# Kernel optimization log

Measured on AMD Instinct MI355X. Metric: run time of the kernel, lower is better.

## Reference

```python
import jax, jax.numpy as jnp
import numpy as np

# Model dims
D = 64          # node channels (dim)
M = 16          # msg_channels
DEPTH = 3
VOCAB = 21      # num_atom_tokens
N = 100000      # nodes
E = 1600000     # directed edges
EIN = 2 * D + 1            # edge_mlp input: [x_i, x_j, |rel|^2]
EH = 2 * EIN               # dim_expansion * edge_input_dim
CH = 4 * M                 # 2 * dim_expansion * msg_channels
NH = 2 * D                 # dim_expansion * in_channels
INIT_STD = 1e-3            # init_eps normal init for Linear weights


def setup_inputs() -> dict:
    key = jax.random.key(0)
    ks = jax.random.split(key, 16)
    feats = jax.random.randint(ks[0], (N,), 0, VOCAB, dtype=jnp.int32)
    coors = jax.random.normal(ks[1], (N, 3), dtype=jnp.float32) * 10.0
    edge_index = jax.random.randint(ks[2], (2, E), 0, N, dtype=jnp.int32)
    emb = jax.random.normal(ks[3], (VOCAB, D), dtype=jnp.float32) * 0.1
    f32 = jnp.float32
    return {
        "feats": feats, "coors": coors, "edge_index": edge_index, "emb": emb,
        # edge_mlp: Linear(EIN->EH), SiLU, Linear(EH->M), SiLU
        "We1": jax.random.normal(ks[4], (DEPTH, EIN, EH), f32) * INIT_STD,
        "be1": jnp.zeros((DEPTH, EH), f32),
        "We2": jax.random.normal(ks[5], (DEPTH, EH, M), f32) * INIT_STD,
        "be2": jnp.zeros((DEPTH, M), f32),
        # coord_mlp: Linear(M->CH), SiLU, Linear(CH->1)
        "Wc1": jax.random.normal(ks[6], (DEPTH, M, CH), f32) * INIT_STD,
        "bc1": jnp.zeros((DEPTH, CH), f32),
        "Wc2": jax.random.normal(ks[7], (DEPTH, CH, 1), f32) * INIT_STD,
        "bc2": jnp.zeros((DEPTH, 1), f32),
        # node_mlp: Linear(D+M->NH), SiLU, Linear(NH->D)
        "Wn1": jax.random.normal(ks[8], (DEPTH, D + M, NH), f32) * INIT_STD,
        "bn1": jnp.zeros((DEPTH, NH), f32),
        "Wn2": jax.random.normal(ks[9], (DEPTH, NH, D), f32) * INIT_STD,
        "bn2": jnp.zeros((DEPTH, D), f32),
    }


def reference(feats, coors, edge_index, emb,
              We1, be1, We2, be2, Wc1, bc1, Wc2, bc2, Wn1, bn1, Wn2, bn2):
    # node_encoder: embedding lookup
    x = emb[feats]                       # [N, D]
    pos = coors                          # [N, 3]
    src = edge_index[0]                  # x_j / pos_j (source, flow source->target)
    tgt = edge_index[1]                  # x_i / pos_i (target) = scatter index
    n = x.shape[0]
    for l in range(DEPTH):
        # message: per-edge gather + MLPs
        rel = pos[tgt] - pos[src]                              # [E, 3]
        d2 = jnp.sum(rel * rel, axis=1, keepdims=True)         # [E, 1]
        m_in = jnp.concatenate([x[tgt], x[src], d2], axis=1)   # [E, 2D+1]
        h = jax.nn.silu(m_in @ We1[l] + be1[l])                # [E, EH]
        msg = jax.nn.silu(h @ We2[l] + be2[l])                 # [E, M]
        cw = jax.nn.silu(msg @ Wc1[l] + bc1[l]) @ Wc2[l] + bc2[l]  # [E, 1]
        pos_msg = rel * cw                                     # [E, 3] (coors_norm is Identity)
        # aggregate: scatter-add to target nodes
        agg_msg = jax.ops.segment_sum(msg, tgt, num_segments=n)      # [N, M]
        agg_pos = jax.ops.segment_sum(pos_msg, tgt, num_segments=n)  # [N, 3]
        # node update: node_norm is Identity
        nh = jax.nn.silu(jnp.concatenate([x, agg_msg], axis=1) @ Wn1[l] + bn1[l])
        out_x = nh @ Wn2[l] + bn2[l]                           # [N, D]
        pos = pos + agg_pos                                    # out_pos += pos (no velocity)
        x = x + out_x                                          # residual=True
    return x, pos
```

## Files before the change

### kernel.cpp

```cpp
#include <hip/hip_runtime.h>
#include <hip/hip_bf16.h>
#include <stdint.h>

#define NDIM   64
#define MDIM   16
#define NLAYER 3
#define EIN    129
#define EHD    258
#define CHD    64
#define NHD    128
#define NIN    80
#define AB_STRIDE 512
#define PKT_STRIDE 32
#define FP8_SCALE 1024.0f
#define NVALS  19

#define WE1F_L (34*2*512)
#define WN1F_L (8*3*512)
#define WN2F_L (4*4*512)
#define WE2F_L (9*512)
#define WC1F_L (4*512)

typedef float vf2 __attribute__((ext_vector_type(2)));
typedef __bf16 bf16x8 __attribute__((ext_vector_type(8)));
typedef float  f32x4  __attribute__((ext_vector_type(4)));

#define MFMA16(a, b, c) __builtin_amdgcn_mfma_f32_16x16x32_bf16((a), (b), (c), 0, 0, 0)

__device__ __forceinline__ float rcp_f(float x) { return __builtin_amdgcn_rcpf(x); }
#if __has_builtin(__builtin_amdgcn_exp2f)
__device__ __forceinline__ float exp2_f(float x) { return __builtin_amdgcn_exp2f(x); }
#else
__device__ __forceinline__ float exp2_f(float x) { return __expf(x * 0.6931471805599453f); }
#endif
__device__ __forceinline__ float silu_f(float v) {
    return v * rcp_f(1.0f + __expf(-v));
}
#define CC_EXP (-1.4426950408889634f / 1024.0f)
__device__ __forceinline__ float hprime_f(float u) {
    return u * rcp_f(1.0f + exp2_f(CC_EXP * u));
}
__device__ __forceinline__ float bflo(uint32_t u) {
    union { uint32_t u; float f; } c; c.u = u << 16; return c.f;
}
__device__ __forceinline__ float bfhi(uint32_t u) {
    union { uint32_t u; float f; } c; c.u = u & 0xffff0000u; return c.f;
}
__device__ __forceinline__ uint32_t pk_fp8_4(float f0, float f1, float f2, float f3) {
    uint32_t r = (uint32_t)__builtin_amdgcn_cvt_pk_fp8_f32(f0, f1, 0, false);
    r = (uint32_t)__builtin_amdgcn_cvt_pk_fp8_f32(f2, f3, (int)r, true);
    return r;
}
__device__ __forceinline__ float clamp8(float v) {
    return fminf(448.0f, fmaxf(-448.0f, v * FP8_SCALE));
}

__global__ void prep_kernel(const float* __restrict__ We1, const float* __restrict__ Wn1,
                            const float* __restrict__ Wn2, const float* __restrict__ We2,
                            const float* __restrict__ Wc1,
                            __bf16* __restrict__ WE1F, __bf16* __restrict__ WN1F,
                            __bf16* __restrict__ WN2F, __bf16* __restrict__ WE2F,
                            __bf16* __restrict__ WC1F) {
    int idx = blockIdx.x * 256 + threadIdx.x;
    const int T1 = NLAYER * WE1F_L;
    if (idx < T1) {
        int l  = idx / WE1F_L;
        int r  = idx % WE1F_L;
        int ct = r / 1024;
        int r2 = r % 1024;
        int kh = r2 / 512;
        int r3 = r2 % 512;
        int lane = r3 >> 3, jj = r3 & 7;
        int half = ct / 17, ctl = ct % 17;
        int col = ctl * 16 + (lane & 15);
        int k = kh * 32 + (lane >> 4) * 8 + jj;
        float v = 0.f;
        if (col < EHD) v = We1[((size_t)l * EIN + (half ? 64 + k : k)) * EHD + col];
        WE1F[idx] = (__bf16)v;
        return;
    }
    idx -= T1;
    const int T2 = NLAYER * WN1F_L;
    if (idx < T2) {
        int l  = idx / WN1F_L;
        int r  = idx % WN1F_L;
        int ct = r / 1536;
        int r2 = r % 1536;
        int kt = r2 / 512;
        int r3 = r2 % 512;
        int lane = r3 >> 3, jj = r3 & 7;
        int col = ct * 16 + (lane & 15);
        int k = kt * 32 + (lane >> 4) * 8 + jj;
        float v = (k < NIN) ? Wn1[((size_t)l * NIN + k) * NHD + col] : 0.f;
        WN1F[idx] = (__bf16)v;
        return;
    }
    idx -= T2;
    const int T3 = NLAYER * WN2F_L;
    if (idx < T3) {
        int l  = idx / WN2F_L;
        int r  = idx % WN2F_L;
        int ct = r / 2048;
        int r2 = r % 2048;
        int kt = r2 / 512;
        int r3 = r2 % 512;
        int lane = r3 >> 3, jj = r3 & 7;
        int col = ct * 16 + (lane & 15);
        int k = kt * 32 + (lane >> 4) * 8 + jj;
        WN2F[idx] = (__bf16)Wn2[((size_t)l * NHD + k) * NDIM + col];
        return;
    }
    idx -= T3;
    const int T4 = NLAYER * WE2F_L;
    if (idx < T4) {
        int l  = idx / WE2F_L;
        int r  = idx % WE2F_L;
        int kt = r / 512;
        int r3 = r % 512;
        int lane = r3 >> 3, jj = r3 & 7;
        int m = lane & 15;
        int k = kt * 32 + (lane >> 4) * 8 + jj;
        float v = (k < EHD) ? We2[((size_t)l * EHD + k) * MDIM + m] * (1.0f / FP8_SCALE) : 0.f;
        WE2F[idx] = (__bf16)v;
        return;
    }
    idx -= T4;
    const int T5 = NLAYER * WC1F_L;
    if (idx < T5) {
        int l  = idx / WC1F_L;
        int r  = idx % WC1F_L;
        int ct = r / 512;
        int r3 = r % 512;
        int lane = r3 >> 3, jj = r3 & 7;
        int c = ct * 16 + (lane & 15);
        int k = (lane >> 4) * 8 + jj;
        float v = (k < MDIM) ? Wc1[((size_t)l * MDIM + k) * CHD + c] : 0.f;
        WC1F[idx] = (__bf16)v;
    }
}

__global__ void init_kernel(const int* __restrict__ feats, const float* __restrict__ coors,
                            const float* __restrict__ emb,
                            float* __restrict__ x, float* __restrict__ pos, int N) {
    int idx = blockIdx.x * 256 + threadIdx.x;
    int nx = N * NDIM;
    if (idx < nx) {
        int n = idx >> 6, c = idx & 63;
        x[idx] = emb[feats[n] * NDIM + c];
    } else {
        int j = idx - nx;
        if (j < N * 3) pos[j] = coors[j];
    }
}

__global__ void hist_kernel(const int* __restrict__ ei, int* __restrict__ cnt, int E) {
    int e = blockIdx.x * 256 + threadIdx.x;
    if (e < E) atomicAdd(&cnt[ei[E + e]], 1);
}

__global__ void scan_sum_kernel(const int* __restrict__ cnt, int* __restrict__ bsum, int N) {
    __shared__ int ws[4];
    int i = blockIdx.x * 256 + threadIdx.x;
    int v = (i < N) ? cnt[i] : 0;
    #pragma unroll
    for (int off = 32; off; off >>= 1) v += __shfl_down(v, off);
    int lane = threadIdx.x & 63, w = threadIdx.x >> 6;
    if (lane == 0) ws[w] = v;
    __syncthreads();
    if (threadIdx.x == 0) bsum[blockIdx.x] = ws[0] + ws[1] + ws[2] + ws[3];
}
__global__ void __launch_bounds__(1024) scan_top_kernel(int* __restrict__ bsum, int nb) {
    __shared__ int ws[16];
    int tid = threadIdx.x, lane = tid & 63, w = tid >> 6;
    int v = (tid < nb) ? bsum[tid] : 0;
    int sc = v;
    #pragma unroll
    for (int off = 1; off < 64; off <<= 1) {
        int u = __shfl_up(sc, off);
        if (lane >= off) sc += u;
    }
    if (lane == 63) ws[w] = sc;
    __syncthreads();
    int woff = 0;
    #pragma unroll
    for (int k = 0; k < 16; ++k) woff += (k < w) ? ws[k] : 0;
    if (tid < nb) bsum[tid] = woff + sc - v;
}
__global__ void scan_fin_kernel(const int* __restrict__ cnt, const int* __restrict__ bsum,
                                int* __restrict__ cursor, int N) {
    __shared__ int ws[4];
    int i = blockIdx.x * 256 + threadIdx.x;
    int tid = threadIdx.x, lane = tid & 63, w = tid >> 6;
    int v = (i < N) ? cnt[i] : 0;
    int sc = v;
    #pragma unroll
    for (int off = 1; off < 64; off <<= 1) {
        int u = __shfl_up(sc, off);
        if (lane >= off) sc += u;
    }
    if (lane == 63) ws[w] = sc;
    __syncthreads();
    int woff = 0;
    #pragma unroll
    for (int k = 0; k < 4; ++k) woff += (k < w) ? ws[k] : 0;
    if (i < N) cursor[i] = bsum[blockIdx.x] + woff + sc - v;
}

__global__ void scatter_kernel(const int* __restrict__ ei, int* __restrict__ cursor,
                               uint2* __restrict__ sorted_st, int E) {
    int e = blockIdx.x * 256 + threadIdx.x;
    if (e >= E) return;
    int s = ei[e], t = ei[E + e];
    int p = atomicAdd(&cursor[t], 1);
    uint2 st; st.x = (uint32_t)s; st.y = (uint32_t)t;
    sorted_st[p] = st;
}

__global__ void __launch_bounds__(256) gemm_ab_mfma(
        const float* __restrict__ x, const float* __restrict__ pos,
        const bf16x8* __restrict__ WE1Fl, const float* __restrict__ be1l,
        uint8_t* __restrict__ A8, uint8_t* __restrict__ pkt,
        float* __restrict__ agg_msg, float* __restrict__ agg_pos, int N) {
    __shared__ __align__(16) __bf16 stg[4][16][280];
    int wave = threadIdx.x >> 6, lane = threadIdx.x & 63;
    int half = wave & 1;
    int nb = blockIdx.x * 32 + (wave >> 1) * 16;
    int lrow = lane & 15, lkg = lane >> 4;
    int row = nb + lrow; if (row >= N) row = N - 1;

    const float* xr = x + (size_t)row * NDIM + lkg * 8;
    bf16x8 a0, a1;
    #pragma unroll
    for (int j = 0; j < 8; ++j) { a0[j] = (__bf16)xr[j]; a1[j] = (__bf16)xr[32 + j]; }

    f32x4 acc[17];
    #pragma unroll
    for (int t = 0; t < 17; ++t) acc[t] = (f32x4){0.f, 0.f, 0.f, 0.f};
    const bf16x8* bf = WE1Fl + (size_t)(half * 17) * 2 * 64 + lane;
    #pragma unroll
    for (int t = 0; t < 17; ++t) {
        bf16x8 b0 = bf[(t * 2 + 0) * 64];
        bf16x8 b1 = bf[(t * 2 + 1) * 64];
        acc[t] = MFMA16(a0, b0, acc[t]);
        acc[t] = MFMA16(a1, b1, acc[t]);
    }
    #pragma unroll
    for (int t = 0; t < 17; ++t) {
        int col = t * 16 + lrow;
        float bias = (half == 0 && col < EHD) ? be1l[col] : 0.f;
        #pragma unroll
        for (int r = 0; r < 4; ++r)
            stg[wave][lkg * 4 + r][col] = (__bf16)(acc[t][r] + bias);
    }
    __syncthreads();

    int node = lane >> 2;
    int gnode = nb + node;
    const __bf16* hrow = &stg[wave][node][(lane & 3) * 64];
    if (gnode < N) {
        uint8_t* dst = A8 + (size_t)gnode * AB_STRIDE + half * 256 + (lane & 3) * 64;
        #pragma unroll
        for (int g = 0; g < 8; ++g) {
            bf16x8 hv = *(const bf16x8*)(hrow + g * 8);
            uint2 pk;
            pk.x = pk_fp8_4(clamp8((float)hv[0]), clamp8((float)hv[1]),
                            clamp8((float)hv[2]), clamp8((float)hv[3]));
            pk.y = pk_fp8_4(clamp8((float)hv[4]), clamp8((float)hv[5]),
                            clamp8((float)hv[6]), clamp8((float)hv[7]));
            *(uint2*)(dst + g * 8) = pk;
        }
    }
    if (lane < 16 && nb + lane < N) {
        int gn = nb + lane;
        const uint16_t* hr = (const uint16_t*)&stg[wave][lane][256];
        uint32_t ex = (uint32_t)hr[0] | ((uint32_t)hr[1] << 16);
        uint32_t* pk = (uint32_t*)(pkt + (size_t)gn * PKT_STRIDE);
        if (half == 0) {
            uint4 w0;
            w0.x = __float_as_uint(pos[3 * gn]);
            w0.y = __float_as_uint(pos[3 * gn + 1]);
            w0.z = __float_as_uint(pos[3 * gn + 2]);
            w0.w = ex;
            *(uint4*)pk = w0;
        } else {
            pk[4] = ex;
        }
    }
    {
        int i16 = blockIdx.x * 512 + (int)threadIdx.x * 2;
        if (i16 + 1 < N * MDIM) {
            *(vf2*)(agg_msg + i16) = (vf2){0.f, 0.f};
        } else if (i16 < N * MDIM) {
            agg_msg[i16] = 0.f;
        }
        if (threadIdx.x < 96) {
            int ip = blockIdx.x * 96 + (int)threadIdx.x;
            if (ip < N * 3) agg_pos[ip] = 0.f;
        }
    }
}

__global__ void __launch_bounds__(256) gather_ab(
        const int* __restrict__ feats, const float* __restrict__ pos,
        const uint8_t* __restrict__ A8v, const uint8_t* __restrict__ pktv,
        uint8_t* __restrict__ A8, uint8_t* __restrict__ pkt,
        float* __restrict__ agg_msg, float* __restrict__ agg_pos, int N) {
    int nb = blockIdx.x * 8;
    int t = threadIdx.x;
    int node = nb + (t >> 5);
    int chunk = t & 31;
    if (node < N) {
        int tok = feats[node];
        const uint4* src = (const uint4*)(A8v + (size_t)tok * AB_STRIDE);
        uint4* dst = (uint4*)(A8 + (size_t)node * AB_STRIDE);
        dst[chunk] = src[chunk];
    }
    if (t < 128) {
        int i = nb * MDIM + t;
        if (i < N * MDIM) agg_msg[i] = 0.f;
    } else if (t < 152) {
        int i = nb * 3 + (t - 128);
        if (i < N * 3) agg_pos[i] = 0.f;
    } else if (t < 160) {
        int n = nb + (t - 152);
        if (n < N) {
            int tok = feats[n];
            const uint32_t* pv = (const uint32_t*)(pktv + (size_t)tok * PKT_STRIDE);
            uint32_t* pk = (uint32_t*)(pkt + (size_t)n * PKT_STRIDE);
            uint4 w0;
            w0.x = __float_as_uint(pos[3 * n]);
            w0.y = __float_as_uint(pos[3 * n + 1]);
            w0.z = __float_as_uint(pos[3 * n + 2]);
            w0.w = pv[3];
            *(uint4*)pk = w0;
            pk[4] = pv[4];
        }
    }
}

__global__ void __launch_bounds__(256) edge_kernel(
        const uint2* __restrict__ sorted_st,
        const uint8_t* __restrict__ A8, const uint8_t* __restrict__ pkt,
        const bf16x8* __restrict__ WE2Fl, const bf16x8* __restrict__ WC1Fl,
        const float* __restrict__ be2l,
        const float* __restrict__ bc1, const float* __restrict__ Wc2,
        const float* __restrict__ bc2, const float* __restrict__ w128,
        float* __restrict__ agg_msg, float* __restrict__ agg_pos, int E) {

    __shared__ __align__(16) vf2    w128p[132];
    __shared__ __align__(16) __bf16 msg_lds[4][64][24];
    __shared__ int  run_t[4][64];
    __shared__ uint run_se[4][64];

    int tid  = threadIdx.x;
    int wave = tid >> 6, lane = tid & 63;
    int kg   = lane >> 4, lrow = lane & 15;

    int base = blockIdx.x * 256 + wave * 64;
    int eo = base + lane;
    bool active = (eo < E);
    int eoc = active ? eo : (E - 1);
    uint2 st = sorted_st[eoc];
    int s_own = (int)st.x;
    int t_ld  = (int)st.y;
    int t_scan = active ? t_ld : -1;

    const uint32_t* ppt = (const uint32_t*)(pkt + (size_t)t_ld  * PKT_STRIDE);
    const uint32_t* pps = (const uint32_t*)(pkt + (size_t)s_own * PKT_STRIDE);
    uint4 pt0 = *(const uint4*)ppt;
    uint4 ps0 = *(const uint4*)pps;
    uint32_t b2o = pps[4];
    uint32_t a2o = pt0.w;
    float rx = __uint_as_float(pt0.x) - __uint_as_float(ps0.x);
    float ry = __uint_as_float(pt0.y) - __uint_as_float(ps0.y);
    float rz = __uint_as_float(pt0.z) - __uint_as_float(ps0.z);
    float d2o = rx*rx + ry*ry + rz*rz;

    bf16x8 bw[9];
    #pragma unroll
    for (int kt = 0; kt < 9; ++kt) bw[kt] = WE2Fl[kt * 64 + lane];
    bf16x8 bwc[4];
    float bc1r[4], wc2r[4];
    #pragma unroll
    for (int ct = 0; ct < 4; ++ct) {
        bwc[ct]  = WC1Fl[ct * 64 + lane];
        bc1r[ct] = bc1[ct * 16 + lrow];
        wc2r[ct] = Wc2[ct * 16 + lrow];
    }
    float be2m = be2l[lrow];
    float cb2  = bc2[0];

    for (int i = tid; i < 132; i += 256) {
        int k0 = i * 2;
        float lo = (k0     < EHD) ? w128[k0]     * FP8_SCALE : 0.f;
        float hi = (k0 + 1 < EHD) ? w128[k0 + 1] * FP8_SCALE : 0.f;
        w128p[i] = (vf2){lo, hi};
    }
    __syncthreads();

    #pragma unroll
    for (int tt = 0; tt < 4; ++tt) {
        int srcl = tt * 16 + lrow;
        int t_r = __shfl(t_ld, srcl);
        int s_r = __shfl(s_own, srcl);
        float d2r = __shfl(d2o, srcl);
        uint32_t a2r = (uint32_t)__shfl((int)a2o, srcl);
        uint32_t b2r = (uint32_t)__shfl((int)b2o, srcl);
        vf2 d2v = (vf2){d2r, d2r};

        const uint8_t* Ar = A8 + (size_t)t_r * AB_STRIDE + kg * 8;
        const uint8_t* Br = A8 + (size_t)s_r * AB_STRIDE + 256 + kg * 8;

        f32x4 acc = (f32x4){0.f, 0.f, 0.f, 0.f};
        #pragma unroll
        for (int kt = 0; kt < 8; ++kt) {
            uint2 ad = *(const uint2*)(Ar + kt * 32);
            uint2 bd = *(const uint2*)(Br + kt * 32);
            const vf2* wp = &w128p[kt * 16 + kg * 4];
            vf2 u0 = __builtin_amdgcn_cvt_pk_f32_fp8(ad.x, false)
                   + __builtin_amdgcn_cvt_pk_f32_fp8(bd.x, false) + d2v * wp[0];
            vf2 u1 = __builtin_amdgcn_cvt_pk_f32_fp8(ad.x, true)
                   + __builtin_amdgcn_cvt_pk_f32_fp8(bd.x, true)  + d2v * wp[1];
            vf2 u2 = __builtin_amdgcn_cvt_pk_f32_fp8(ad.y, false)
                   + __builtin_amdgcn_cvt_pk_f32_fp8(bd.y, false) + d2v * wp[2];
            vf2 u3 = __builtin_amdgcn_cvt_pk_f32_fp8(ad.y, true)
                   + __builtin_amdgcn_cvt_pk_f32_fp8(bd.y, true)  + d2v * wp[3];
            bf16x8 af;
            af[0] = (__bf16)hprime_f(u0.x); af[1] = (__bf16)hprime_f(u0.y);
            af[2] = (__bf16)hprime_f(u1.x); af[3] = (__bf16)hprime_f(u1.y);
            af[4] = (__bf16)hprime_f(u2.x); af[5] = (__bf16)hprime_f(u2.y);
            af[6] = (__bf16)hprime_f(u3.x); af[7] = (__bf16)hprime_f(u3.y);
            acc = MFMA16(af, bw[kt], acc);
        }
        {
            float h0 = 0.f, h1 = 0.f;
            if (kg == 0) {
                vf2 wx = w128p[128];
                float u0 = (bflo(a2r) + bflo(b2r)) * FP8_SCALE + d2r * wx.x;
                float u1 = (bfhi(a2r) + bfhi(b2r)) * FP8_SCALE + d2r * wx.y;
                h0 = hprime_f(u0);
                h1 = hprime_f(u1);
            }
            bf16x8 af;
            af[0] = (__bf16)h0; af[1] = (__bf16)h1;
            #pragma unroll
            for (int j = 2; j < 8; ++j) af[j] = (__bf16)0.f;
            acc = MFMA16(af, bw[8], acc);
        }
        #pragma unroll
        for (int r = 0; r < 4; ++r) {
            float mval = silu_f(acc[r] + be2m);
            msg_lds[wave][tt * 16 + kg * 4 + r][lrow] = (__bf16)mval;
        }
    }
    __builtin_amdgcn_wave_barrier();

    #pragma unroll
    for (int tt = 0; tt < 4; ++tt) {
        bf16x8 ac = (bf16x8){(__bf16)0.f,(__bf16)0.f,(__bf16)0.f,(__bf16)0.f,
                             (__bf16)0.f,(__bf16)0.f,(__bf16)0.f,(__bf16)0.f};
        if (kg < 2) ac = *(const bf16x8*)&msg_lds[wave][tt * 16 + lrow][kg * 8];
        f32x4 c0 = (f32x4){0.f,0.f,0.f,0.f}, c1 = c0, c2 = c0, c3 = c0;
        c0 = MFMA16(ac, bwc[0], c0);
        c1 = MFMA16(ac, bwc[1], c1);
        c2 = MFMA16(ac, bwc[2], c2);
        c3 = MFMA16(ac, bwc[3], c3);
        float p0 = 0.f, p1 = 0.f, p2 = 0.f, p3 = 0.f;
        p0 += silu_f(c0[0] + bc1r[0]) * wc2r[0]; p1 += silu_f(c0[1] + bc1r[0]) * wc2r[0];
        p2 += silu_f(c0[2] + bc1r[0]) * wc2r[0]; p3 += silu_f(c0[3] + bc1r[0]) * wc2r[0];
        p0 += silu_f(c1[0] + bc1r[1]) * wc2r[1]; p1 += silu_f(c1[1] + bc1r[1]) * wc2r[1];
        p2 += silu_f(c1[2] + bc1r[1]) * wc2r[1]; p3 += silu_f(c1[3] + bc1r[1]) * wc2r[1];
        p0 += silu_f(c2[0] + bc1r[2]) * wc2r[2]; p1 += silu_f(c2[1] + bc1r[2]) * wc2r[2];
        p2 += silu_f(c2[2] + bc1r[2]) * wc2r[2]; p3 += silu_f(c2[3] + bc1r[2]) * wc2r[2];
        p0 += silu_f(c3[0] + bc1r[3]) * wc2r[3]; p1 += silu_f(c3[1] + bc1r[3]) * wc2r[3];
        p2 += silu_f(c3[2] + bc1r[3]) * wc2r[3]; p3 += silu_f(c3[3] + bc1r[3]) * wc2r[3];
        #pragma unroll
        for (int mk = 1; mk < 16; mk <<= 1) {
            p0 += __shfl_xor(p0, mk);
            p1 += __shfl_xor(p1, mk);
            p2 += __shfl_xor(p2, mk);
            p3 += __shfl_xor(p3, mk);
        }
        if (lrow < 4) {
            float sel = (lrow == 0) ? p0 : (lrow == 1) ? p1 : (lrow == 2) ? p2 : p3;
            msg_lds[wave][tt * 16 + kg * 4 + lrow][16] = (__bf16)(cb2 + sel);
        }
    }
    __builtin_amdgcn_wave_barrier();

    float cwo = (float)msg_lds[wave][lane][16];
    msg_lds[wave][lane][16] = (__bf16)(rx * cwo);
    msg_lds[wave][lane][17] = (__bf16)(ry * cwo);
    msg_lds[wave][lane][18] = (__bf16)(rz * cwo);

    int t_next = __shfl_down(t_scan, 1);
    bool is_end = (lane == 63) || (t_next != t_scan);
    uint64_t mask = __ballot(is_end);
    int nr = __popcll(mask);
    if (is_end) {
        uint64_t below = mask & ((1ULL << lane) - 1ULL);
        int rid = __popcll(below);
        int st2 = (below == 0ULL) ? 0 : (64 - __builtin_clzll(below));
        run_t[wave][rid]  = t_scan;
        run_se[wave][rid] = (uint)((st2 << 8) | lane);
    }
    __builtin_amdgcn_wave_barrier();

    for (int task = lane; task < nr * NVALS; task += 64) {
        int rid = task / NVALS;
        int v   = task - rid * NVALS;
        int t   = run_t[wave][rid];
        if (t >= 0) {
            uint se = run_se[wave][rid];
            int st2 = (int)(se >> 8), en = (int)(se & 0xFFu);
            float sum = 0.f;
            for (int e = st2; e <= en; ++e) sum += (float)msg_lds[wave][e][v];
            if (v < 16) atomicAdd(&agg_msg[(size_t)t * MDIM + v], sum);
            else        atomicAdd(&agg_pos[(size_t)t * 3 + (v - 16)], sum);
        }
    }
}

__global__ void __launch_bounds__(256) node_mfma(
        float* __restrict__ x, float* __restrict__ pos,
        const float* __restrict__ agg_msg, const float* __restrict__ agg_pos,
        const bf16x8* __restrict__ WN1Fl, const bf16x8* __restrict__ WN2Fl,
        const float* __restrict__ bn1l, const float* __restrict__ bn2l, int N) {
    __shared__ __align__(16) __bf16 stg[4][16][136];
    int wave = threadIdx.x >> 6, lane = threadIdx.x & 63;
    int nb = blockIdx.x * 64 + wave * 16;
    int lrow = lane & 15, lkg = lane >> 4;
    int row = nb + lrow;
    int rc = (row < N) ? row : (N - 1);

    const float* xr = x + (size_t)rc * NDIM + lkg * 8;
    bf16x8 a0, a1, a2;
    #pragma unroll
    for (int j = 0; j < 8; ++j) { a0[j] = (__bf16)xr[j]; a1[j] = (__bf16)xr[32 + j]; }
    if (lkg < 2) {
        const float* mr = agg_msg + (size_t)rc * MDIM + lkg * 8;
        #pragma unroll
        for (int j = 0; j < 8; ++j) a2[j] = (__bf16)mr[j];
    } else {
        #pragma unroll
        for (int j = 0; j < 8; ++j) a2[j] = (__bf16)0.f;
    }

    f32x4 h[8];
    #pragma unroll
    for (int t = 0; t < 8; ++t) h[t] = (f32x4){0.f, 0.f, 0.f, 0.f};
    const bf16x8* b1 = WN1Fl + lane;
    #pragma unroll
    for (int t = 0; t < 8; ++t) {
        h[t] = MFMA16(a0, b1[(t * 3 + 0) * 64], h[t]);
        h[t] = MFMA16(a1, b1[(t * 3 + 1) * 64], h[t]);
        h[t] = MFMA16(a2, b1[(t * 3 + 2) * 64], h[t]);
    }
    #pragma unroll
    for (int t = 0; t < 8; ++t) {
        int col = t * 16 + lrow;
        float bias = bn1l[col];
        #pragma unroll
        for (int r = 0; r < 4; ++r)
            stg[wave][lkg * 4 + r][col] = (__bf16)silu_f(h[t][r] + bias);
    }
    __syncthreads();

    bf16x8 af[4];
    #pragma unroll
    for (int kt = 0; kt < 4; ++kt)
        af[kt] = *(const bf16x8*)&stg[wave][lrow][kt * 32 + lkg * 8];

    f32x4 o[4];
    #pragma unroll
    for (int t = 0; t < 4; ++t) o[t] = (f32x4){0.f, 0.f, 0.f, 0.f};
    const bf16x8* b2 = WN2Fl + lane;
    #pragma unroll
    for (int t = 0; t < 4; ++t) {
        #pragma unroll
        for (int kt = 0; kt < 4; ++kt)
            o[t] = MFMA16(af[kt], b2[(t * 4 + kt) * 64], o[t]);
    }

    int orow = nb + lkg * 4;
    #pragma unroll
    for (int t = 0; t < 4; ++t) {
        int col = t * 16 + lrow;
        float bias = bn2l[col];
        #pragma unroll
        for (int r = 0; r < 4; ++r) {
            int rr = orow + r;
            if (rr < N) x[(size_t)rr * NDIM + col] += o[t][r] + bias;
        }
    }
    if (threadIdx.x < 192) {
        long j = (long)blockIdx.x * 192 + threadIdx.x;
        if (j < (long)N * 3) pos[j] += agg_pos[j];
    }
}

extern "C" void kernel_launch(void* const* d_in, const int* in_sizes, int n_in,
                              void* d_out, int out_size, void* d_ws, size_t ws_size,
                              hipStream_t stream) {
    const int*   feats = (const int*)  d_in[0];
    const float* coors = (const float*)d_in[1];
    const int*   ei    = (const int*)  d_in[2];
    const float* emb   = (const float*)d_in[3];
    const float* We1   = (const float*)d_in[4];
    const float* be1   = (const float*)d_in[5];
    const float* We2   = (const float*)d_in[6];
    const float* be2   = (const float*)d_in[7];
    const float* Wc1   = (const float*)d_in[8];
    const float* bc1   = (const float*)d_in[9];
    const float* Wc2   = (const float*)d_in[10];
    const float* bc2   = (const float*)d_in[11];
    const float* Wn1   = (const float*)d_in[12];
    const float* bn1   = (const float*)d_in[13];
    const float* Wn2   = (const float*)d_in[14];
    const float* bn2   = (const float*)d_in[15];

    const int N = in_sizes[0];
    const int E = in_sizes[2] / 2;
    const int VOCAB = in_sizes[3] / NDIM;

    float* x   = (float*)d_out;
    float* pos = (float*)d_out + (size_t)N * NDIM;

    char* w = (char*)d_ws;
    uint8_t* A8 = (uint8_t*)w;
    size_t off = ((size_t)N * AB_STRIDE + 255) & ~(size_t)255;
    uint8_t* pkt = (uint8_t*)(w + off);
    off += ((size_t)N * PKT_STRIDE + 255) & ~(size_t)255;
    float* agg_msg = (float*)(w + off);
    off += ((size_t)N * MDIM * 4 + 255) & ~(size_t)255;
    float* agg_pos = (float*)(w + off);
    off += ((size_t)N * 3 * 4 + 255) & ~(size_t)255;
    uint2* sorted_st = (uint2*)(w + off);
    off += ((size_t)E * 8 + 255) & ~(size_t)255;
    int* cnt = (int*)(w + off);
    off += ((size_t)N * 4 + 255) & ~(size_t)255;
    int* cursor = (int*)(w + off);
    off += ((size_t)N * 4 + 255) & ~(size_t)255;
    int* bsum = (int*)(w + off);
    off += (((size_t)N / 256 + 2) * 4 + 255) & ~(size_t)255;
    uint8_t* A8v = (uint8_t*)(w + off);
    off += (size_t)32 * AB_STRIDE;
    uint8_t* pktv = (uint8_t*)(w + off);
    off += (size_t)32 * PKT_STRIDE;
    __bf16* WE1F = (__bf16*)(w + off);
    off += ((size_t)NLAYER * WE1F_L * 2 + 255) & ~(size_t)255;
    __bf16* WN1F = (__bf16*)(w + off);
    off += ((size_t)NLAYER * WN1F_L * 2 + 255) & ~(size_t)255;
    __bf16* WN2F = (__bf16*)(w + off);
    off += ((size_t)NLAYER * WN2F_L * 2 + 255) & ~(size_t)255;
    __bf16* WE2F = (__bf16*)(w + off);
    off += ((size_t)NLAYER * WE2F_L * 2 + 255) & ~(size_t)255;
    __bf16* WC1F = (__bf16*)(w + off);
    (void)ws_size; (void)n_in; (void)out_size;

    {
        int total = NLAYER * (WE1F_L + WN1F_L + WN2F_L + WE2F_L + WC1F_L);
        prep_kernel<<<(total + 255) / 256, 256, 0, stream>>>(We1, Wn1, Wn2, We2, Wc1,
                                                             WE1F, WN1F, WN2F, WE2F, WC1F);
    }
    {
        int total = N * (NDIM + 3);
        init_kernel<<<(total + 255) / 256, 256, 0, stream>>>(feats, coors, emb, x, pos, N);
    }
    hipMemsetAsync(cnt, 0, (size_t)N * 4, stream);
    hist_kernel<<<(E + 255) / 256, 256, 0, stream>>>(ei, cnt, E);
    {
        int nb = (N + 255) / 256;
        scan_sum_kernel<<<nb, 256, 0, stream>>>(cnt, bsum, N);
        scan_top_kernel<<<1, 1024, 0, stream>>>(bsum, nb);
        scan_fin_kernel<<<nb, 256, 0, stream>>>(cnt, bsum, cursor, N);
    }
    scatter_kernel<<<(E + 255) / 256, 256, 0, stream>>>(ei, cursor, sorted_st, E);

    for (int l = 0; l < NLAYER; ++l) {
        const float* We1_l  = We1 + (size_t)l * EIN * EHD;
        const float* w128_l = We1_l + (size_t)128 * EHD;

        if (l == 0) {
            gemm_ab_mfma<<<(VOCAB + 31) / 32, 256, 0, stream>>>(
                emb, pos, (const bf16x8*)(WE1F + (size_t)l * WE1F_L),
                be1 + (size_t)l * EHD, A8v, pktv, agg_msg, agg_pos, VOCAB);
            gather_ab<<<(N + 7) / 8, 256, 0, stream>>>(
                feats, pos, A8v, pktv, A8, pkt, agg_msg, agg_pos, N);
        } else {
            gemm_ab_mfma<<<(N + 31) / 32, 256, 0, stream>>>(
                x, pos, (const bf16x8*)(WE1F + (size_t)l * WE1F_L),
                be1 + (size_t)l * EHD, A8, pkt, agg_msg, agg_pos, N);
        }

        edge_kernel<<<(E + 255) / 256, 256, 0, stream>>>(
            sorted_st, A8, pkt,
            (const bf16x8*)(WE2F + (size_t)l * WE2F_L),
            (const bf16x8*)(WC1F + (size_t)l * WC1F_L),
            be2 + (size_t)l * MDIM,
            bc1 + (size_t)l * CHD, Wc2 + (size_t)l * CHD, bc2 + l, w128_l,
            agg_msg, agg_pos, E);

        node_mfma<<<(N + 63) / 64, 256, 0, stream>>>(
            x, pos, agg_msg, agg_pos,
            (const bf16x8*)(WN1F + (size_t)l * WN1F_L),
            (const bf16x8*)(WN2F + (size_t)l * WN2F_L),
            bn1 + (size_t)l * NHD, bn2 + (size_t)l * NDIM, N);
    }
}
```

Before: 1.118 ms.

## Fuse node MLP update with next layer's edge-input GEMM and accumulator reset

Adds a fused kernel that runs the node MLP and residual update, then immediately computes the next layer's per-node We1 projection (packed to fp8 with position packets) from the freshly updated x in LDS. It also zeroes the aggregation buffers, so the separate gemm_ab_mfma launch for layers 1 and 2 goes away. The aim is to save a launch and a full re-read of x and pos between layers. The edge kernel's two message and coordinate loops are also merged into one per-tile loop with per-iteration wave barriers. The cost is a heavier kernel with high register use (17 accumulators per half) and a block-wide sync, which may lower occupancy.

```diff
diff --git a/kernel.cpp b/kernel.cpp
--- a/kernel.cpp
+++ b/kernel.cpp
@@ -452,11 +452,8 @@
             float mval = silu_f(acc[r] + be2m);
             msg_lds[wave][tt * 16 + kg * 4 + r][lrow] = (__bf16)mval;
         }
-    }
-    __builtin_amdgcn_wave_barrier();
-
-    #pragma unroll
-    for (int tt = 0; tt < 4; ++tt) {
+        __builtin_amdgcn_wave_barrier();
+
         bf16x8 ac = (bf16x8){(__bf16)0.f,(__bf16)0.f,(__bf16)0.f,(__bf16)0.f,
                              (__bf16)0.f,(__bf16)0.f,(__bf16)0.f,(__bf16)0.f};
         if (kg < 2) ac = *(const bf16x8*)&msg_lds[wave][tt * 16 + lrow][kg * 8];
@@ -485,8 +482,8 @@
             float sel = (lrow == 0) ? p0 : (lrow == 1) ? p1 : (lrow == 2) ? p2 : p3;
             msg_lds[wave][tt * 16 + kg * 4 + lrow][16] = (__bf16)(cb2 + sel);
         }
-    }
-    __builtin_amdgcn_wave_barrier();
+        __builtin_amdgcn_wave_barrier();
+    }
 
     float cwo = (float)msg_lds[wave][lane][16];
     msg_lds[wave][lane][16] = (__bf16)(rx * cwo);
@@ -596,6 +593,167 @@
     if (threadIdx.x < 192) {
         long j = (long)blockIdx.x * 192 + threadIdx.x;
         if (j < (long)N * 3) pos[j] += agg_pos[j];
+    }
+}
+
+__global__ void __launch_bounds__(256) node_gemm_fused(
+        float* __restrict__ x, float* __restrict__ pos,
+        const float* __restrict__ agg_msg, const float* __restrict__ agg_pos,
+        const bf16x8* __restrict__ WN1Fl, const bf16x8* __restrict__ WN2Fl,
+        const float* __restrict__ bn1l, const float* __restrict__ bn2l,
+        const bf16x8* __restrict__ WE1Fn, const float* __restrict__ be1n,
+        uint8_t* __restrict__ A8, uint8_t* __restrict__ pkt, int N) {
+    __shared__ __align__(16) __bf16 stg[4][16][280];
+    int wave = threadIdx.x >> 6, lane = threadIdx.x & 63;
+    int nb = blockIdx.x * 64 + wave * 16;
+    int lrow = lane & 15, lkg = lane >> 4;
+    int row = nb + lrow;
+    int rc = (row < N) ? row : (N - 1);
+
+    const float* xr = x + (size_t)rc * NDIM + lkg * 8;
+    bf16x8 a0, a1, a2;
+    #pragma unroll
+    for (int j = 0; j < 8; ++j) { a0[j] = (__bf16)xr[j]; a1[j] = (__bf16)xr[32 + j]; }
+    if (lkg < 2) {
+        const float* mr = agg_msg + (size_t)rc * MDIM + lkg * 8;
+        #pragma unroll
+        for (int j = 0; j < 8; ++j) a2[j] = (__bf16)mr[j];
+    } else {
+        #pragma unroll
+        for (int j = 0; j < 8; ++j) a2[j] = (__bf16)0.f;
+    }
+
+    f32x4 h[8];
+    #pragma unroll
+    for (int t = 0; t < 8; ++t) h[t] = (f32x4){0.f, 0.f, 0.f, 0.f};
+    const bf16x8* b1 = WN1Fl + lane;
+    #pragma unroll
+    for (int t = 0; t < 8; ++t) {
+        h[t] = MFMA16(a0, b1[(t * 3 + 0) * 64], h[t]);
+        h[t] = MFMA16(a1, b1[(t * 3 + 1) * 64], h[t]);
+        h[t] = MFMA16(a2, b1[(t * 3 + 2) * 64], h[t]);
+    }
+    #pragma unroll
+    for (int t = 0; t < 8; ++t) {
+        int col = t * 16 + lrow;
+        float bias = bn1l[col];
+        #pragma unroll
+        for (int r = 0; r < 4; ++r)
+            stg[wave][lkg * 4 + r][col] = (__bf16)silu_f(h[t][r] + bias);
+    }
+    __builtin_amdgcn_wave_barrier();
+
+    bf16x8 af[4];
+    #pragma unroll
+    for (int kt = 0; kt < 4; ++kt)
+        af[kt] = *(const bf16x8*)&stg[wave][lrow][kt * 32 + lkg * 8];
+
+    f32x4 o[4];
+    #pragma unroll
+    for (int t = 0; t < 4; ++t) o[t] = (f32x4){0.f, 0.f, 0.f, 0.f};
+    const bf16x8* b2 = WN2Fl + lane;
+    #pragma unroll
+    for (int t = 0; t < 4; ++t) {
+        #pragma unroll
+        for (int kt = 0; kt < 4; ++kt)
+            o[t] = MFMA16(af[kt], b2[(t * 4 + kt) * 64], o[t]);
+    }
+    __builtin_amdgcn_wave_barrier();
+
+    int orow = nb + lkg * 4;
+    #pragma unroll
+    for (int t = 0; t < 4; ++t) {
+        int col = t * 16 + lrow;
+        float bias = bn2l[col];
+        #pragma unroll
+        for (int r = 0; r < 4; ++r) {
+            int rr = orow + r;
+            int rrc = (rr < N) ? rr : (N - 1);
+            float xv = x[(size_t)rrc * NDIM + col] + o[t][r] + bias;
+            if (rr < N) x[(size_t)rr * NDIM + col] = xv;
+            stg[wave][lkg * 4 + r][col] = (__bf16)xv;
+        }
+    }
+    if (threadIdx.x < 192) {
+        long j = (long)blockIdx.x * 192 + threadIdx.x;
+        if (j < (long)N * 3) pos[j] += agg_pos[j];
+    }
+    __syncthreads();
+
+    bf16x8 g0 = *(const bf16x8*)&stg[wave][lrow][lkg * 8];
+    bf16x8 g1 = *(const bf16x8*)&stg[wave][lrow][32 + lkg * 8];
+    __builtin_amdgcn_wave_barrier();
+
+    int node = lane >> 2;
+    int gnode = nb + node;
+    #pragma unroll
+    for (int half = 0; half < 2; ++half) {
+        f32x4 acc[17];
+        #pragma unroll
+        for (int t = 0; t < 17; ++t) acc[t] = (f32x4){0.f, 0.f, 0.f, 0.f};
+        const bf16x8* bf = WE1Fn + (size_t)(half * 17) * 2 * 64 + lane;
+        #pragma unroll
+        for (int t = 0; t < 17; ++t) {
+            bf16x8 b0 = bf[(t * 2 + 0) * 64];
+            bf16x8 bb1 = bf[(t * 2 + 1) * 64];
+            acc[t] = MFMA16(g0, b0, acc[t]);
+            acc[t] = MFMA16(g1, bb1, acc[t]);
+        }
+        #pragma unroll
+        for (int t = 0; t < 17; ++t) {
+            int col = t * 16 + lrow;
+            float bias = (half == 0 && col < EHD) ? be1n[col] : 0.f;
+            #pragma unroll
+            for (int r = 0; r < 4; ++r)
+                stg[wave][lkg * 4 + r][col] = (__bf16)(acc[t][r] + bias);
+        }
+        __builtin_amdgcn_wave_barrier();
+
+        const __bf16* hrow = &stg[wave][node][(lane & 3) * 64];
+        if (gnode < N) {
+            uint8_t* dst = A8 + (size_t)gnode * AB_STRIDE + half * 256 + (lane & 3) * 64;
+            #pragma unroll
+            for (int g = 0; g < 8; ++g) {
+                bf16x8 hv = *(const bf16x8*)(hrow + g * 8);
+                uint2 pk;
+                pk.x = pk_fp8_4(clamp8((float)hv[0]), clamp8((float)hv[1]),
+                                clamp8((float)hv[2]), clamp8((float)hv[3]));
+                pk.y = pk_fp8_4(clamp8((float)hv[4]), clamp8((float)hv[5]),
+                                clamp8((float)hv[6]), clamp8((float)hv[7]));
+                *(uint2*)(dst + g * 8) = pk;
+            }
+        }
+        if (lane < 16 && nb + lane < N) {
+            int gn = nb + lane;
+            const uint16_t* hr = (const uint16_t*)&stg[wave][lane][256];
+            uint32_t ex = (uint32_t)hr[0] | ((uint32_t)hr[1] << 16);
+            uint32_t* pk = (uint32_t*)(pkt + (size_t)gn * PKT_STRIDE);
+            if (half == 0) {
+                uint4 w0;
+                w0.x = __float_as_uint(pos[3 * gn]);
+                w0.y = __float_as_uint(pos[3 * gn + 1]);
+                w0.z = __float_as_uint(pos[3 * gn + 2]);
+                w0.w = ex;
+                *(uint4*)pk = w0;
+            } else {
+                pk[4] = ex;
+            }
+        }
+        __builtin_amdgcn_wave_barrier();
+    }
+
+    {
+        long i16 = (long)blockIdx.x * 1024 + (long)threadIdx.x * 4;
+        if (i16 + 3 < (long)N * MDIM) {
+            *(f32x4*)(agg_msg + i16) = (f32x4){0.f, 0.f, 0.f, 0.f};
+        } else {
+            for (int q = 0; q < 4; ++q)
+                if (i16 + q < (long)N * MDIM) ((float*)agg_msg)[i16 + q] = 0.f;
+        }
+        if (threadIdx.x < 192) {
+            long ip = (long)blockIdx.x * 192 + threadIdx.x;
+            if (ip < (long)N * 3) ((float*)agg_pos)[ip] = 0.f;
+        }
     }
 }
 
@@ -677,21 +835,14 @@
     }
     scatter_kernel<<<(E + 255) / 256, 256, 0, stream>>>(ei, cursor, sorted_st, E);
 
+    gemm_ab_mfma<<<(VOCAB + 31) / 32, 256, 0, stream>>>(
+        emb, pos, (const bf16x8*)WE1F, be1, A8v, pktv, agg_msg, agg_pos, VOCAB);
+    gather_ab<<<(N + 7) / 8, 256, 0, stream>>>(
+        feats, pos, A8v, pktv, A8, pkt, agg_msg, agg_pos, N);
+
     for (int l = 0; l < NLAYER; ++l) {
         const float* We1_l  = We1 + (size_t)l * EIN * EHD;
         const float* w128_l = We1_l + (size_t)128 * EHD;
-
-        if (l == 0) {
-            gemm_ab_mfma<<<(VOCAB + 31) / 32, 256, 0, stream>>>(
-                emb, pos, (const bf16x8*)(WE1F + (size_t)l * WE1F_L),
-                be1 + (size_t)l * EHD, A8v, pktv, agg_msg, agg_pos, VOCAB);
-            gather_ab<<<(N + 7) / 8, 256, 0, stream>>>(
-                feats, pos, A8v, pktv, A8, pkt, agg_msg, agg_pos, N);
-        } else {
-            gemm_ab_mfma<<<(N + 31) / 32, 256, 0, stream>>>(
-                x, pos, (const bf16x8*)(WE1F + (size_t)l * WE1F_L),
-                be1 + (size_t)l * EHD, A8, pkt, agg_msg, agg_pos, N);
-        }
 
         edge_kernel<<<(E + 255) / 256, 256, 0, stream>>>(
             sorted_st, A8, pkt,
@@ -701,10 +852,21 @@
             bc1 + (size_t)l * CHD, Wc2 + (size_t)l * CHD, bc2 + l, w128_l,
             agg_msg, agg_pos, E);
 
-        node_mfma<<<(N + 63) / 64, 256, 0, stream>>>(
-            x, pos, agg_msg, agg_pos,
-            (const bf16x8*)(WN1F + (size_t)l * WN1F_L),
-            (const bf16x8*)(WN2F + (size_t)l * WN2F_L),
-            bn1 + (size_t)l * NHD, bn2 + (size_t)l * NDIM, N);
-    }
-}
+        if (l < NLAYER - 1) {
+            node_gemm_fused<<<(N + 63) / 64, 256, 0, stream>>>(
+                x, pos, agg_msg, agg_pos,
+                (const bf16x8*)(WN1F + (size_t)l * WN1F_L),
+                (const bf16x8*)(WN2F + (size_t)l * WN2F_L),
+                bn1 + (size_t)l * NHD, bn2 + (size_t)l * NDIM,
+                (const bf16x8*)(WE1F + (size_t)(l + 1) * WE1F_L),
+                be1 + (size_t)(l + 1) * EHD,
+                A8, pkt, N);
+        } else {
+            node_mfma<<<(N + 63) / 64, 256, 0, stream>>>(
+                x, pos, agg_msg, agg_pos,
+                (const bf16x8*)(WN1F + (size_t)l * WN1F_L),
+                (const bf16x8*)(WN2F + (size_t)l * WN2F_L),
+                bn1 + (size_t)l * NHD, bn2 + (size_t)l * NDIM, N);
+        }
+    }
+}
```

After: 986.7 us. 11.7% less time.
